# Kernel tuning notes

Measured on AMD Instinct MI355X. Metric: run time of the kernel, lower is better.

## Reference

```python
import jax, jax.numpy as jnp
import numpy as np

N = 50000; E = 800000; T = 800000; G = 64
H = 128; IEMB = 128; BAS = 8; NS = 4; NR = 6; OEH = 128; OUT = 1; NB = 4; CUT = 5.0


def envelope(x):
    # exponent=5 -> p=6: 1/x + a*x^5 + b*x^6 + c*x^7 with a=-28, b=48, c=-21
    return 1.0 / x - 28.0 * x**5 + 48.0 * x**6 - 21.0 * x**7


def setup_inputs() -> dict:
    key = jax.random.key(0)
    ks = iter(jax.random.split(key, 80))
    def w(shape, s=0.1):
        return jax.random.normal(next(ks), shape, dtype=jnp.float32) * s
    inp = {}
    inp['z'] = jax.random.randint(next(ks), (N,), 0, 100, dtype=jnp.int32)
    inp['dist'] = jax.random.uniform(next(ks), (E,), jnp.float32, 0.05, 1.0)
    inp['dist_trip'] = jax.random.uniform(next(ks), (T,), jnp.float32, 0.05, 1.0)
    inp['angle'] = jax.random.uniform(next(ks), (T,), jnp.float32, -1.0, 1.0)
    inp['edge_index'] = jax.random.randint(next(ks), (2, E), 0, N, dtype=jnp.int32)
    inp['triplets'] = jax.random.randint(next(ks), (T, 3), 0, N, dtype=jnp.int32)
    inp['batch'] = jnp.sort(jax.random.randint(next(ks), (N,), 0, G, dtype=jnp.int32))
    inp['atom_table'] = w((100, H), 1.0)
    inp['rbf_freq'] = jnp.arange(1, NR + 1, dtype=jnp.float32) * jnp.float32(np.pi)
    inp['sbf_freq'] = jnp.arange(1, NR + 1, dtype=jnp.float32) * jnp.float32(np.pi)
    inp['emb_w1'] = w((NR, IEMB)); inp['emb_b1'] = w((IEMB,), 0.01)
    inp['emb_w2'] = w((IEMB, H)); inp['emb_b2'] = w((H,), 0.01)
    inp['iw_rbf1'] = w((NB, NR, BAS)); inp['iw_rbf2'] = w((NB, BAS, H))
    inp['iw_sbf1'] = w((NB, NS * NR, BAS)); inp['iw_sbf2'] = w((NB, BAS, IEMB))
    inp['iw_t1'] = w((NB, H, IEMB)); inp['iw_t2'] = w((NB, IEMB, H)); inp['ib_t2'] = w((NB, H), 0.01)
    inp['iw_up'] = w((NB, H, H)); inp['ib_up'] = w((NB, H), 0.01)
    inp['iw_down'] = w((NB, H, H)); inp['ib_down'] = w((NB, H), 0.01)
    inp['ow_rbf'] = w((NB + 1, NR, H))
    inp['ow0'] = w((NB + 1, H, OEH)); inp['ob0'] = w((NB + 1, OEH), 0.01)
    inp['ow1'] = w((NB + 1, OEH, OEH)); inp['ob1'] = w((NB + 1, OEH), 0.01)
    inp['ow2'] = w((NB + 1, OEH, OUT)); inp['ob2'] = w((NB + 1, OUT), 0.01)
    return inp


def _forward(atom_table, rbf_freq, sbf_freq, emb_w1, emb_b1, emb_w2, emb_b2,
             iw_rbf1, iw_rbf2, iw_sbf1, iw_sbf2, iw_t1, iw_t2, ib_t2,
             iw_up, ib_up, iw_down, ib_down, ow_rbf, ow0, ob0, ow1, ob1, ow2, ob2,
             dist, dist_trip, angle, z, edge_index, triplets, batch):
    row, col = edge_index[0], edge_index[1]
    j_idx = triplets[:, 1]
    # radial basis for edges: [E, NR]
    d = dist[:, None] / CUT
    rbf_e = envelope(d) * jnp.sin(rbf_freq * d)
    # spherical basis for triplets: [T, NS*NR]
    dt = dist_trip[:, None] / CUT
    rbf_t = envelope(dt) * jnp.sin(sbf_freq * dt)
    a = angle[:, None]
    sph = jnp.concatenate([jnp.ones_like(a), a, 0.5 * (3 * a**2 - 1), 0.5 * (5 * a**3 - 3 * a)], axis=-1)
    sbf_t = (rbf_t[:, None, :] * sph[:, :, None]).reshape(a.shape[0], -1)

    x = atom_table[z]  # [N, H]
    # EmbeddingBlock: edge msg from rbf only, scattered to col
    e = jax.nn.silu(rbf_e @ emb_w1 + emb_b1) @ emb_w2 + emb_b2
    x = x + jax.ops.segment_sum(e, col, num_segments=N)

    def out_block(k, x):
        rbf_emb = rbf_e @ ow_rbf[k]            # [E, H]
        h = jax.ops.segment_sum(x[row] * rbf_emb, col, num_segments=N)
        h = jax.nn.silu(h @ ow0[k] + ob0[k])
        h = jax.nn.silu(h @ ow1[k] + ob1[k])
        return h @ ow2[k] + ob2[k]             # [N, OUT]

    P = out_block(0, x)
    for b in range(NB):
        x_up = x @ iw_up[b] + ib_up[b]
        x_down = x @ iw_down[b] + ib_down[b]
        rbf_emb = jax.nn.silu(rbf_e @ iw_rbf1[b]) @ iw_rbf2[b]      # [E, H]
        x_edge = x_up[row] * rbf_emb                                  # [E, H]
        sbf_emb = jax.nn.silu(sbf_t @ iw_sbf1[b]) @ iw_sbf2[b]      # [T, H]
        t = jax.nn.silu(x_down @ iw_t1[b]) @ iw_t2[b] + ib_t2[b]     # [N, H]
        # original: for each triplet i, x_edge += t[j]*sbf_emb[i] (broadcast over all edges)
        extra = jnp.sum(t[j_idx] * sbf_emb, axis=0)                   # [H]
        x_edge = x_edge + extra
        x = x + jax.ops.segment_sum(x_edge, col, num_segments=N)
        P = P + out_block(b + 1, x)

    counts = jax.ops.segment_sum(jnp.ones((x.shape[0],), jnp.float32), batch, num_segments=G)
    pooled = jax.ops.segment_sum(P, batch, num_segments=G) / jnp.maximum(counts, 1.0)[:, None]
    return pooled  # [G, OUT]


def reference(z, dist, dist_trip, angle, edge_index, triplets, batch, atom_table, rbf_freq, sbf_freq,
              emb_w1, emb_b1, emb_w2, emb_b2, iw_rbf1, iw_rbf2, iw_sbf1, iw_sbf2, iw_t1, iw_t2, ib_t2,
              iw_up, ib_up, iw_down, ib_down, ow_rbf, ow0, ob0, ow1, ob1, ow2, ob2):
    return _forward(atom_table, rbf_freq, sbf_freq, emb_w1, emb_b1, emb_w2, emb_b2,
                    iw_rbf1, iw_rbf2, iw_sbf1, iw_sbf2, iw_t1, iw_t2, ib_t2,
                    iw_up, ib_up, iw_down, ib_down, ow_rbf, ow0, ob0, ow1, ob1, ow2, ob2,
                    dist, dist_trip, angle, z, edge_index, triplets, batch)
```

## Files before the change

### kernel.cpp

```cpp
#include <hip/hip_runtime.h>
#include <hip/hip_fp16.h>

#define N_ 50000
#define E_ 800000
#define T_ 800000
#define G_ 64
#define H_ 128

#define NBK 782
#define NSB (NBK * 8)
#define CAPS 512

typedef __attribute__((ext_vector_type(8))) short bf16x8;
typedef __attribute__((ext_vector_type(4))) float f32x4;
typedef _Float16 f16x2 __attribute__((ext_vector_type(2)));

__device__ __forceinline__ float siluf(float v) {
    return __fdividef(v, 1.0f + __expf(-v));
}

__device__ __forceinline__ unsigned short f2bf(float f) {
    unsigned int u = __float_as_uint(f);
    u += 0x7fffu + ((u >> 16) & 1u);
    return (unsigned short)(u >> 16);
}
__device__ __forceinline__ unsigned int f2bf2(float a, float b) {
    return (unsigned int)f2bf(a) | ((unsigned int)f2bf(b) << 16);
}
__device__ __forceinline__ float bf2f(unsigned short h) {
    return __uint_as_float(((unsigned int)h) << 16);
}
__device__ __forceinline__ float2 bf2x2(unsigned int p) {
    return make_float2(__uint_as_float(p << 16), __uint_as_float(p & 0xffff0000u));
}
__device__ __forceinline__ float fdot2f(f16x2 a, f16x2 b, float c) {
    return __builtin_amdgcn_fdot2(a, b, c, false);
}

__global__ __launch_bounds__(256) void k_bucket(const int* __restrict__ ecol, const int* __restrict__ erow,
                                                const float* __restrict__ dist,
                                                const int* __restrict__ trip,
                                                const float* __restrict__ dist_trip, const float* __restrict__ angle,
                                                int* bcntE, int2* __restrict__ ebktP, unsigned char* __restrict__ ebktC,
                                                int* bcntT, float2* __restrict__ tbktP, unsigned char* __restrict__ tbktC) {
    int i = blockIdx.x * 256 + threadIdx.x;
    int r = blockIdx.x & 7;
    if (i < E_) {
        int col = ecol[i];
        int sb = (col >> 6) * 8 + r;
        int pos = atomicAdd(&bcntE[sb], 1);
        if (pos < CAPS) {
            ebktP[(size_t)sb * CAPS + pos] = make_int2(erow[i], __float_as_int(dist[i]));
            ebktC[(size_t)sb * CAPS + pos] = (unsigned char)(col & 63);
        }
    }
    int t = i - E_;
    if (t >= 0 && t < T_) {
        int j = trip[3 * t + 1];
        int sb = (j >> 6) * 8 + r;
        int pos = atomicAdd(&bcntT[sb], 1);
        if (pos < CAPS) {
            tbktP[(size_t)sb * CAPS + pos] = make_float2(dist_trip[t], angle[t]);
            tbktC[(size_t)sb * CAPS + pos] = (unsigned char)(j & 63);
        }
    }
}

__global__ __launch_bounds__(256) void k_cnt(const int* __restrict__ bcntE, const unsigned char* __restrict__ ebktC,
                                             const int* __restrict__ bcntT, const unsigned char* __restrict__ tbktC,
                                             int* __restrict__ degE, int* __restrict__ degT) {
    int b = blockIdx.x;
    bool isE = b < NBK;
    if (!isE) b -= NBK;
    __shared__ int c[64];
    int tid = threadIdx.x;
    if (tid < 64) c[tid] = 0;
    __syncthreads();
    const int* bcnt = isE ? bcntE : bcntT;
    const unsigned char* bc = isE ? ebktC : tbktC;
    for (int s = 0; s < 8; ++s) {
        int sb = b * 8 + s;
        int nb = min(bcnt[sb], CAPS);
        for (int i = tid; i < nb; i += 256) atomicAdd(&c[bc[(size_t)sb * CAPS + i]], 1);
    }
    __syncthreads();
    if (tid < 64) {
        int col = b * 64 + tid;
        if (col < N_) (isE ? degE : degT)[col] = c[tid];
    }
}

__global__ __launch_bounds__(1024) void k_scan2(const int* __restrict__ degE, int* rowptrE, int* curE,
                                                const int* __restrict__ degT, int* rowptrT, int* curT, int n) {
    const int* deg = (blockIdx.x == 0) ? degE : degT;
    int* rowptr = (blockIdx.x == 0) ? rowptrE : rowptrT;
    int* cur = (blockIdx.x == 0) ? curE : curT;
    __shared__ int wsum[16];
    __shared__ int s_carry;
    int tid = threadIdx.x, lane = tid & 63, w = tid >> 6;
    if (tid == 0) s_carry = 0;
    __syncthreads();
    for (int base = 0; base < n; base += 1024) {
        int i = base + tid;
        int v = (i < n) ? deg[i] : 0;
        int incl = v;
        #pragma unroll
        for (int s = 1; s < 64; s <<= 1) {
            int t = __shfl_up(incl, (unsigned)s, 64);
            if (lane >= s) incl += t;
        }
        if (lane == 63) wsum[w] = incl;
        __syncthreads();
        int carry0 = s_carry;
        int wexcl = 0;
        for (int j = 0; j < w; ++j) wexcl += wsum[j];
        int excl = carry0 + wexcl + (incl - v);
        if (i < n) { rowptr[i] = excl; cur[i] = excl; }
        __syncthreads();
        if (tid == 1023) s_carry = carry0 + wexcl + incl;
        __syncthreads();
    }
    if (tid == 0) rowptr[n] = s_carry;
}

__global__ __launch_bounds__(256) void k_place(const int* __restrict__ bcntE, const int2* __restrict__ ebktP,
                                               const unsigned char* __restrict__ ebktC, int* curE,
                                               int* __restrict__ slist, float* __restrict__ distS,
                                               const int* __restrict__ bcntT, const float2* __restrict__ tbktP,
                                               const unsigned char* __restrict__ tbktC, int* curT,
                                               float2* __restrict__ tpay) {
    int b = blockIdx.x;
    bool isE = b < NBK;
    if (!isE) b -= NBK;
    int tid = threadIdx.x;
    if (isE) {
        for (int s = 0; s < 8; ++s) {
            int sb = b * 8 + s;
            int nb = min(bcntE[sb], CAPS);
            for (int i = tid; i < nb; i += 256) {
                size_t idx = (size_t)sb * CAPS + i;
                int col = b * 64 + ebktC[idx];
                int2 pr = ebktP[idx];
                int pos = atomicAdd(&curE[col], 1);
                slist[pos] = pr.x;
                distS[pos] = __int_as_float(pr.y);
            }
        }
    } else {
        for (int s = 0; s < 8; ++s) {
            int sb = b * 8 + s;
            int nb = min(bcntT[sb], CAPS);
            for (int i = tid; i < nb; i += 256) {
                size_t idx = (size_t)sb * CAPS + i;
                int col = b * 64 + tbktC[idx];
                float2 pr = tbktP[idx];
                int pos = atomicAdd(&curT[col], 1);
                tpay[pos] = pr;
            }
        }
    }
}

__global__ __launch_bounds__(256) void k_wprep(const float* __restrict__ emb_w2, const float* __restrict__ iw_down,
                                               const float* __restrict__ iw_t1, const float* __restrict__ iw_t2,
                                               const float* __restrict__ iw_up, const float* __restrict__ ow0,
                                               const float* __restrict__ ow1, unsigned short* __restrict__ Wt) {
    int mat = blockIdx.x >> 3;
    int part = blockIdx.x & 7;
    const float* src;
    if (mat == 0) src = emb_w2;
    else if (mat < 5) src = iw_down + (size_t)(mat - 1) * 16384;
    else if (mat < 9) src = iw_t1 + (size_t)(mat - 5) * 16384;
    else if (mat < 13) src = iw_t2 + (size_t)(mat - 9) * 16384;
    else if (mat < 17) src = iw_up + (size_t)(mat - 13) * 16384;
    else if (mat < 22) src = ow0 + (size_t)(mat - 17) * 16384;
    else src = ow1 + (size_t)(mat - 22) * 16384;
    unsigned short* dst = Wt + (size_t)mat * 16384;
    int base = part * 2048;
    for (int i = base + threadIdx.x; i < base + 2048; i += 256) {
        int k = i >> 7, n = i & 127;
        dst[n * 128 + k] = f2bf(src[i]);
    }
}

__global__ __launch_bounds__(256) void k_geom(const float* __restrict__ distS,
                                              const float* __restrict__ freq, const float* __restrict__ iw_rbf1,
                                              float* __restrict__ rbfS, __half* __restrict__ s8all, int n) {
    __shared__ float W1s[4][48];
    int tid = threadIdx.x;
    if (tid < 192) W1s[tid / 48][tid % 48] = iw_rbf1[tid];
    __syncthreads();
    int p = blockIdx.x * 256 + tid;
    if (p >= n) return;
    float d = distS[p] * 0.2f;
    float d2 = d * d, d4 = d2 * d2, d5 = d4 * d;
    float env = __fdividef(1.0f, d) - 28.0f * d5 + 48.0f * d5 * d - 21.0f * d5 * d2;
    float rb[6];
    #pragma unroll
    for (int r = 0; r < 6; ++r) {
        rb[r] = env * __sinf(freq[r] * d);
        rbfS[(size_t)p * 6 + r] = rb[r];
    }
    #pragma unroll
    for (int b = 0; b < 4; ++b) {
        __half out[8];
        #pragma unroll
        for (int k = 0; k < 8; ++k) {
            float u = 0.f;
            #pragma unroll
            for (int r = 0; r < 6; ++r) u += rb[r] * W1s[b][r * 8 + k];
            out[k] = __float2half(siluf(u));
        }
        *(uint4*)&s8all[((size_t)b * n + p) * 8] = *(uint4*)out;
    }
}

__global__ __launch_bounds__(256) void k_basis(const float2* __restrict__ tpay,
                                               const float* __restrict__ sfreq, __half* __restrict__ basis, int n) {
    int t = blockIdx.x * 256 + threadIdx.x;
    if (t >= n) return;
    float2 da = tpay[t];
    float d = da.x * 0.2f;
    float a = da.y;
    float d2 = d * d, d4 = d2 * d2, d5 = d4 * d;
    float env = __fdividef(1.0f, d) - 28.0f * d5 + 48.0f * d5 * d - 21.0f * d5 * d2;
    float rb[6];
    #pragma unroll
    for (int r = 0; r < 6; ++r) rb[r] = env * __sinf(sfreq[r] * d);
    float sph[4];
    sph[0] = 1.0f; sph[1] = a; sph[2] = 1.5f * a * a - 0.5f; sph[3] = 2.5f * a * a * a - 1.5f * a;
    __half out[24];
    #pragma unroll
    for (int s = 0; s < 4; ++s)
        #pragma unroll
        for (int r = 0; r < 6; ++r) out[s * 6 + r] = __float2half(sph[s] * rb[r]);
    uint4* dst = (uint4*)(basis + (size_t)t * 24);
    dst[0] = ((uint4*)out)[0];
    dst[1] = ((uint4*)out)[1];
    dst[2] = ((uint4*)out)[2];
}

__global__ __launch_bounds__(256) void k_sv4(const int* __restrict__ rowptrT, const __half* __restrict__ basis,
                                             const float* __restrict__ iw_sbf1, float* __restrict__ SV4, int n) {
    int wave = threadIdx.x >> 6, lane = threadIdx.x & 63;
    int node = blockIdx.x * 8 + wave * 2 + (lane >> 5);
    int sub = lane & 31;
    int blk = sub >> 3, k = sub & 7;
    if (node >= n) return;
    const float* W1 = iw_sbf1 + blk * 192;
    f16x2 w[12];
    #pragma unroll
    for (int j = 0; j < 12; ++j) {
        f16x2 t;
        t.x = (_Float16)W1[(2 * j) * 8 + k];
        t.y = (_Float16)W1[(2 * j + 1) * 8 + k];
        w[j] = t;
    }
    float acc = 0.f;
    int p0 = rowptrT[node], p1 = rowptrT[node + 1];
    for (int p = p0; p < p1; ++p) {
        union { uint4 q[3]; f16x2 h[12]; } bs;
        const uint4* bp = (const uint4*)(basis + (size_t)p * 24);
        bs.q[0] = bp[0]; bs.q[1] = bp[1]; bs.q[2] = bp[2];
        float u = 0.f;
        #pragma unroll
        for (int j = 0; j < 12; ++j) u = fdot2f(bs.h[j], w[j], u);
        acc += siluf(u);
    }
    SV4[((size_t)blk * n + node) * 8 + k] = acc;
}

__global__ __launch_bounds__(256) void k_init_x(const float* __restrict__ atab, const int* __restrict__ z,
                                                unsigned short* __restrict__ xh, int n) {
    int t = blockIdx.x * 256 + threadIdx.x;
    if (t >= n * 16) return;
    int node = t >> 4, q = t & 15;
    const float4* a4 = (const float4*)atab;
    float4 v0 = a4[(size_t)z[node] * 32 + q * 2];
    float4 v1 = a4[(size_t)z[node] * 32 + q * 2 + 1];
    uint4 pk;
    pk.x = f2bf2(v0.x, v0.y);
    pk.y = f2bf2(v0.z, v0.w);
    pk.z = f2bf2(v1.x, v1.y);
    pk.w = f2bf2(v1.z, v1.w);
    ((uint4*)xh)[t] = pk;
}

__global__ __launch_bounds__(256) void k_embS(const int* __restrict__ rowptr, const float* __restrict__ rbfS,
                                              const float* __restrict__ w1, const float* __restrict__ b1,
                                              float* __restrict__ SS, int n) {
    int node = blockIdx.x * 4 + (threadIdx.x >> 6);
    int lane = threadIdx.x & 63;
    if (node >= n) return;
    int c = lane * 2;
    float wc0[6], wc1[6];
    #pragma unroll
    for (int r = 0; r < 6; ++r) { wc0[r] = w1[r * 128 + c]; wc1[r] = w1[r * 128 + c + 1]; }
    float bb0 = b1[c], bb1 = b1[c + 1];
    float a0 = 0.f, a1 = 0.f;
    int p0 = rowptr[node], p1 = rowptr[node + 1];
    for (int p = p0; p < p1; ++p) {
        const float2* r2 = (const float2*)&rbfS[(size_t)p * 6];
        float2 ra = r2[0], rbx = r2[1], rc = r2[2];
        float u0 = bb0 + ra.x * wc0[0] + ra.y * wc0[1] + rbx.x * wc0[2] + rbx.y * wc0[3] + rc.x * wc0[4] + rc.y * wc0[5];
        float u1 = bb1 + ra.x * wc1[0] + ra.y * wc1[1] + rbx.x * wc1[2] + rbx.y * wc1[3] + rc.x * wc1[4] + rc.y * wc1[5];
        a0 += siluf(u0);
        a1 += siluf(u1);
    }
    SS[node * 128 + c] = a0;
    SS[node * 128 + c + 1] = a1;
}

template <int BIAS_MODE, bool SILU, bool ACCBF, bool ABF, bool WF32, bool WBF>
__global__ __launch_bounds__(256, 4) void k_gemm_mfma(const void* __restrict__ Ap,
                                                      const unsigned short* __restrict__ Wt,
                                                      const float* __restrict__ bias, const int* __restrict__ deg,
                                                      float* __restrict__ C, unsigned short* __restrict__ Ch, int M) {
    int tid = threadIdx.x;
    int wave = tid >> 6, lane = tid & 63;
    int m15 = lane & 15, quad = lane >> 4;
    int row0 = blockIdx.x * 64 + wave * 16;
    int arow = row0 + m15;
    if (arow > M - 1) arow = M - 1;

    f32x4 acc[8];
    #pragma unroll
    for (int nt = 0; nt < 8; ++nt) acc[nt] = (f32x4){0.f, 0.f, 0.f, 0.f};

    #pragma unroll
    for (int kt = 0; kt < 4; ++kt) {
        int ks = kt * 32 + quad * 8;
        bf16x8 av;
        if constexpr (ABF) {
            av = *(const bf16x8*)((const unsigned short*)Ap + (size_t)arow * 128 + ks);
        } else {
            const float* Arow = (const float*)Ap + (size_t)arow * 128;
            float4 a0 = *(const float4*)(Arow + ks);
            float4 a1 = *(const float4*)(Arow + ks + 4);
            union { bf16x8 v; unsigned int u[4]; } af;
            af.u[0] = f2bf2(a0.x, a0.y);
            af.u[1] = f2bf2(a0.z, a0.w);
            af.u[2] = f2bf2(a1.x, a1.y);
            af.u[3] = f2bf2(a1.z, a1.w);
            av = af.v;
        }
        #pragma unroll
        for (int nt = 0; nt < 8; ++nt) {
            bf16x8 bf = *(const bf16x8*)(Wt + (size_t)(nt * 16 + m15) * 128 + ks);
            acc[nt] = __builtin_amdgcn_mfma_f32_16x16x32_bf16(av, bf, acc[nt], 0, 0, 0);
        }
    }

    #pragma unroll
    for (int nt = 0; nt < 8; ++nt) {
        int col = nt * 16 + m15;
        float bc = 0.f;
        if constexpr (BIAS_MODE != 0) bc = bias[col];
        #pragma unroll
        for (int reg = 0; reg < 4; ++reg) {
            int row = row0 + quad * 4 + reg;
            if (row < M) {
                float v = acc[nt][reg];
                if constexpr (BIAS_MODE == 1) v += bc;
                if constexpr (BIAS_MODE == 2) v += bc * (float)deg[row];
                if constexpr (SILU) v = siluf(v);
                if constexpr (ACCBF) v += bf2f(Ch[(size_t)row * 128 + col]);
                if constexpr (WF32) C[(size_t)row * 128 + col] = v;
                if constexpr (WBF) Ch[(size_t)row * 128 + col] = f2bf(v);
            }
        }
    }
}

template <int PACC>
__global__ __launch_bounds__(256, 4) void k_out_mlp(const unsigned short* __restrict__ hB,
                                                    const unsigned short* __restrict__ W0t, const float* __restrict__ b0,
                                                    const unsigned short* __restrict__ W1t, const float* __restrict__ b1,
                                                    const float* __restrict__ w2col, const float* __restrict__ ob2p,
                                                    float* __restrict__ Pout, int M) {
    __shared__ unsigned short lds[4][16 * 136];
    int tid = threadIdx.x;
    int wave = tid >> 6, lane = tid & 63;
    int m15 = lane & 15, quad = lane >> 4;
    int row0 = blockIdx.x * 64 + wave * 16;
    int arow = row0 + m15;
    if (arow > M - 1) arow = M - 1;
    unsigned short* L = lds[wave];

    f32x4 acc[8];
    #pragma unroll
    for (int nt = 0; nt < 8; ++nt) acc[nt] = (f32x4){0.f, 0.f, 0.f, 0.f};
    #pragma unroll
    for (int kt = 0; kt < 4; ++kt) {
        int ks = kt * 32 + quad * 8;
        bf16x8 av = *(const bf16x8*)(hB + (size_t)arow * 128 + ks);
        #pragma unroll
        for (int nt = 0; nt < 8; ++nt) {
            bf16x8 bf = *(const bf16x8*)(W0t + (size_t)(nt * 16 + m15) * 128 + ks);
            acc[nt] = __builtin_amdgcn_mfma_f32_16x16x32_bf16(av, bf, acc[nt], 0, 0, 0);
        }
    }
    #pragma unroll
    for (int nt = 0; nt < 8; ++nt) {
        int col = nt * 16 + m15;
        float bc = b0[col];
        #pragma unroll
        for (int reg = 0; reg < 4; ++reg)
            L[(quad * 4 + reg) * 136 + col] = f2bf(siluf(acc[nt][reg] + bc));
    }
    __syncthreads();

    #pragma unroll
    for (int nt = 0; nt < 8; ++nt) acc[nt] = (f32x4){0.f, 0.f, 0.f, 0.f};
    #pragma unroll
    for (int kt = 0; kt < 4; ++kt) {
        int ks = kt * 32 + quad * 8;
        bf16x8 av = *(const bf16x8*)(L + m15 * 136 + ks);
        #pragma unroll
        for (int nt = 0; nt < 8; ++nt) {
            bf16x8 bf = *(const bf16x8*)(W1t + (size_t)(nt * 16 + m15) * 128 + ks);
            acc[nt] = __builtin_amdgcn_mfma_f32_16x16x32_bf16(av, bf, acc[nt], 0, 0, 0);
        }
    }
    float w2c[8], pp[4];
    #pragma unroll
    for (int nt = 0; nt < 8; ++nt) w2c[nt] = w2col[nt * 16 + m15];
    #pragma unroll
    for (int reg = 0; reg < 4; ++reg) pp[reg] = 0.f;
    #pragma unroll
    for (int nt = 0; nt < 8; ++nt) {
        float bc = b1[nt * 16 + m15];
        #pragma unroll
        for (int reg = 0; reg < 4; ++reg)
            pp[reg] += siluf(acc[nt][reg] + bc) * w2c[nt];
    }
    #pragma unroll
    for (int reg = 0; reg < 4; ++reg) {
        float s = pp[reg];
        s += __shfl_xor(s, 1, 64);
        s += __shfl_xor(s, 2, 64);
        s += __shfl_xor(s, 4, 64);
        s += __shfl_xor(s, 8, 64);
        if (m15 == 0) {
            int row = row0 + quad * 4 + reg;
            if (row < M) {
                float r = s + ob2p[0];
                if constexpr (PACC == 2) r += Pout[row];
                Pout[row] = r;
            }
        }
    }
}

__global__ __launch_bounds__(256, 4) void k_block_mlp(const unsigned short* __restrict__ xh,
                                                      const unsigned short* __restrict__ Wd, const float* __restrict__ bd,
                                                      const unsigned short* __restrict__ Wt1,
                                                      const unsigned short* __restrict__ Wt2, const float* __restrict__ bt2,
                                                      const unsigned short* __restrict__ Wup, const float* __restrict__ bup,
                                                      float* __restrict__ Tm, unsigned short* __restrict__ xuph, int M) {
    __shared__ unsigned short lds[4][16 * 136];
    int tid = threadIdx.x;
    int wave = tid >> 6, lane = tid & 63;
    int m15 = lane & 15, quad = lane >> 4;
    int row0 = blockIdx.x * 64 + wave * 16;
    int arow = row0 + m15;
    if (arow > M - 1) arow = M - 1;
    unsigned short* L = lds[wave];

    f32x4 accD[8], accU[8];
    #pragma unroll
    for (int nt = 0; nt < 8; ++nt) { accD[nt] = (f32x4){0.f, 0.f, 0.f, 0.f}; accU[nt] = (f32x4){0.f, 0.f, 0.f, 0.f}; }
    #pragma unroll
    for (int kt = 0; kt < 4; ++kt) {
        int ks = kt * 32 + quad * 8;
        bf16x8 av = *(const bf16x8*)(xh + (size_t)arow * 128 + ks);
        #pragma unroll
        for (int nt = 0; nt < 8; ++nt) {
            bf16x8 bd_ = *(const bf16x8*)(Wd + (size_t)(nt * 16 + m15) * 128 + ks);
            accD[nt] = __builtin_amdgcn_mfma_f32_16x16x32_bf16(av, bd_, accD[nt], 0, 0, 0);
            bf16x8 bu_ = *(const bf16x8*)(Wup + (size_t)(nt * 16 + m15) * 128 + ks);
            accU[nt] = __builtin_amdgcn_mfma_f32_16x16x32_bf16(av, bu_, accU[nt], 0, 0, 0);
        }
    }
    #pragma unroll
    for (int nt = 0; nt < 8; ++nt) {
        int col = nt * 16 + m15;
        float bcu = bup[col], bcd = bd[col];
        #pragma unroll
        for (int reg = 0; reg < 4; ++reg) {
            int row = row0 + quad * 4 + reg;
            if (row < M) xuph[(size_t)row * 128 + col] = f2bf(accU[nt][reg] + bcu);
            L[(quad * 4 + reg) * 136 + col] = f2bf(accD[nt][reg] + bcd);
        }
    }
    __syncthreads();

    #pragma unroll
    for (int nt = 0; nt < 8; ++nt) accD[nt] = (f32x4){0.f, 0.f, 0.f, 0.f};
    #pragma unroll
    for (int kt = 0; kt < 4; ++kt) {
        int ks = kt * 32 + quad * 8;
        bf16x8 av = *(const bf16x8*)(L + m15 * 136 + ks);
        #pragma unroll
        for (int nt = 0; nt < 8; ++nt) {
            bf16x8 bf = *(const bf16x8*)(Wt1 + (size_t)(nt * 16 + m15) * 128 + ks);
            accD[nt] = __builtin_amdgcn_mfma_f32_16x16x32_bf16(av, bf, accD[nt], 0, 0, 0);
        }
    }
    __syncthreads();
    #pragma unroll
    for (int nt = 0; nt < 8; ++nt) {
        int col = nt * 16 + m15;
        #pragma unroll
        for (int reg = 0; reg < 4; ++reg)
            L[(quad * 4 + reg) * 136 + col] = f2bf(siluf(accD[nt][reg]));
    }
    __syncthreads();

    #pragma unroll
    for (int nt = 0; nt < 8; ++nt) accD[nt] = (f32x4){0.f, 0.f, 0.f, 0.f};
    #pragma unroll
    for (int kt = 0; kt < 4; ++kt) {
        int ks = kt * 32 + quad * 8;
        bf16x8 av = *(const bf16x8*)(L + m15 * 136 + ks);
        #pragma unroll
        for (int nt = 0; nt < 8; ++nt) {
            bf16x8 bf = *(const bf16x8*)(Wt2 + (size_t)(nt * 16 + m15) * 128 + ks);
            accD[nt] = __builtin_amdgcn_mfma_f32_16x16x32_bf16(av, bf, accD[nt], 0, 0, 0);
        }
    }
    #pragma unroll
    for (int nt = 0; nt < 8; ++nt) {
        int col = nt * 16 + m15;
        float bc = bt2[col];
        #pragma unroll
        for (int reg = 0; reg < 4; ++reg) {
            int row = row0 + quad * 4 + reg;
            if (row < M) Tm[(size_t)row * 128 + col] = accD[nt][reg] + bc;
        }
    }
}

__global__ __launch_bounds__(256) void k_out_gather(const int* __restrict__ rowptr, const int* __restrict__ slist,
                                                    const float* __restrict__ rbfS,
                                                    const unsigned short* __restrict__ xh,
                                                    const float* __restrict__ wrbf,
                                                    unsigned short* __restrict__ hB, int n) {
    int node = blockIdx.x * 4 + (threadIdx.x >> 6);
    int lane = threadIdx.x & 63;
    if (node >= n) return;
    int c = lane * 2;
    float wc0[6], wc1[6];
    #pragma unroll
    for (int r = 0; r < 6; ++r) { wc0[r] = wrbf[r * 128 + c]; wc1[r] = wrbf[r * 128 + c + 1]; }
    float a0 = 0.f, a1 = 0.f;
    int p0 = rowptr[node], p1 = rowptr[node + 1];
    int p = p0;
    for (; p + 4 <= p1; p += 4) {
        int s0 = slist[p], s1 = slist[p + 1], s2 = slist[p + 2], s3 = slist[p + 3];
        float2 rb[4][3];
        #pragma unroll
        for (int u = 0; u < 4; ++u) {
            const float2* r2 = (const float2*)&rbfS[(size_t)(p + u) * 6];
            rb[u][0] = r2[0]; rb[u][1] = r2[1]; rb[u][2] = r2[2];
        }
        unsigned int xv0 = *(const unsigned int*)&xh[(size_t)s0 * 128 + c];
        unsigned int xv1 = *(const unsigned int*)&xh[(size_t)s1 * 128 + c];
        unsigned int xv2 = *(const unsigned int*)&xh[(size_t)s2 * 128 + c];
        unsigned int xv3 = *(const unsigned int*)&xh[(size_t)s3 * 128 + c];
        #pragma unroll
        for (int u = 0; u < 4; ++u) {
            float e0 = rb[u][0].x * wc0[0] + rb[u][0].y * wc0[1] + rb[u][1].x * wc0[2] +
                       rb[u][1].y * wc0[3] + rb[u][2].x * wc0[4] + rb[u][2].y * wc0[5];
            float e1 = rb[u][0].x * wc1[0] + rb[u][0].y * wc1[1] + rb[u][1].x * wc1[2] +
                       rb[u][1].y * wc1[3] + rb[u][2].x * wc1[4] + rb[u][2].y * wc1[5];
            float2 xf = bf2x2((u == 0) ? xv0 : (u == 1) ? xv1 : (u == 2) ? xv2 : xv3);
            a0 += xf.x * e0;
            a1 += xf.y * e1;
        }
    }
    for (; p < p1; ++p) {
        int src = slist[p];
        const float2* r2 = (const float2*)&rbfS[(size_t)p * 6];
        float2 ra = r2[0], rbx = r2[1], rc = r2[2];
        float e0 = ra.x * wc0[0] + ra.y * wc0[1] + rbx.x * wc0[2] + rbx.y * wc0[3] + rc.x * wc0[4] + rc.y * wc0[5];
        float e1 = ra.x * wc1[0] + ra.y * wc1[1] + rbx.x * wc1[2] + rbx.y * wc1[3] + rc.x * wc1[4] + rc.y * wc1[5];
        float2 xf = bf2x2(*(const unsigned int*)&xh[(size_t)src * 128 + c]);
        a0 += xf.x * e0;
        a1 += xf.y * e1;
    }
    *(unsigned int*)&hB[(size_t)node * 128 + c] = f2bf2(a0, a1);
}

__global__ __launch_bounds__(256) void k_extra_fused(const float* __restrict__ Tm, const float* __restrict__ SV,
                                                     const float* __restrict__ W2, float* __restrict__ extra, int n) {
    int tid = threadIdx.x;
    int c = tid & 127, half = tid >> 7;
    float acc[8];
    #pragma unroll
    for (int k = 0; k < 8; ++k) acc[k] = 0.f;
    for (int nn = blockIdx.x * 2 + half; nn < n; nn += gridDim.x * 2) {
        const float4* sv4 = (const float4*)&SV[(size_t)nn * 8];
        float4 s0 = sv4[0], s1 = sv4[1];
        float t = Tm[(size_t)nn * 128 + c];
        acc[0] += t * s0.x; acc[1] += t * s0.y; acc[2] += t * s0.z; acc[3] += t * s0.w;
        acc[4] += t * s1.x; acc[5] += t * s1.y; acc[6] += t * s1.z; acc[7] += t * s1.w;
    }
    float e = 0.f;
    #pragma unroll
    for (int k = 0; k < 8; ++k) e += acc[k] * W2[k * 128 + c];
    __shared__ float red[256];
    red[tid] = e;
    __syncthreads();
    if (tid < 128) atomicAdd(&extra[c], red[tid] + red[tid + 128]);
}

__global__ __launch_bounds__(256) void k_interact(const int* __restrict__ rowptr, const int* __restrict__ slist,
                                                  const __half* __restrict__ s8, const float* __restrict__ W2,
                                                  const float* __restrict__ extra,
                                                  const unsigned short* __restrict__ xuph,
                                                  unsigned short* __restrict__ xh, int n) {
    int node = blockIdx.x * 4 + (threadIdx.x >> 6);
    int lane = threadIdx.x & 63;
    if (node >= n) return;
    int c = lane * 2;
    f16x2 w2a[4], w2b[4];
    #pragma unroll
    for (int j = 0; j < 4; ++j) {
        f16x2 wa, wb;
        wa.x = (_Float16)W2[(2 * j) * 128 + c];
        wa.y = (_Float16)W2[(2 * j + 1) * 128 + c];
        wb.x = (_Float16)W2[(2 * j) * 128 + c + 1];
        wb.y = (_Float16)W2[(2 * j + 1) * 128 + c + 1];
        w2a[j] = wa;
        w2b[j] = wb;
    }
    int p0 = rowptr[node], p1 = rowptr[node + 1];
    float cntf = (float)(p1 - p0);
    float a0 = cntf * extra[c], a1 = cntf * extra[c + 1];
    int p = p0;
    for (; p + 4 <= p1; p += 4) {
        int s0 = slist[p], s1 = slist[p + 1], s2 = slist[p + 2], s3 = slist[p + 3];
        uint4 sv[4];
        #pragma unroll
        for (int u = 0; u < 4; ++u) sv[u] = *(const uint4*)(s8 + (size_t)(p + u) * 8);
        unsigned int xv0 = *(const unsigned int*)&xuph[(size_t)s0 * 128 + c];
        unsigned int xv1 = *(const unsigned int*)&xuph[(size_t)s1 * 128 + c];
        unsigned int xv2 = *(const unsigned int*)&xuph[(size_t)s2 * 128 + c];
        unsigned int xv3 = *(const unsigned int*)&xuph[(size_t)s3 * 128 + c];
        #pragma unroll
        for (int u = 0; u < 4; ++u) {
            union { uint4 q; f16x2 h[4]; } s;
            s.q = sv[u];
            float e0 = fdot2f(s.h[0], w2a[0], 0.f);
            e0 = fdot2f(s.h[1], w2a[1], e0);
            e0 = fdot2f(s.h[2], w2a[2], e0);
            e0 = fdot2f(s.h[3], w2a[3], e0);
            float e1 = fdot2f(s.h[0], w2b[0], 0.f);
            e1 = fdot2f(s.h[1], w2b[1], e1);
            e1 = fdot2f(s.h[2], w2b[2], e1);
            e1 = fdot2f(s.h[3], w2b[3], e1);
            float2 xf = bf2x2((u == 0) ? xv0 : (u == 1) ? xv1 : (u == 2) ? xv2 : xv3);
            a0 += xf.x * e0;
            a1 += xf.y * e1;
        }
    }
    for (; p < p1; ++p) {
        int src = slist[p];
        float2 xf = bf2x2(*(const unsigned int*)&xuph[(size_t)src * 128 + c]);
        union { uint4 q; f16x2 h[4]; } s;
        s.q = *(const uint4*)(s8 + (size_t)p * 8);
        float e0 = fdot2f(s.h[0], w2a[0], 0.f);
        e0 = fdot2f(s.h[1], w2a[1], e0);
        e0 = fdot2f(s.h[2], w2a[2], e0);
        e0 = fdot2f(s.h[3], w2a[3], e0);
        float e1 = fdot2f(s.h[0], w2b[0], 0.f);
        e1 = fdot2f(s.h[1], w2b[1], e1);
        e1 = fdot2f(s.h[2], w2b[2], e1);
        e1 = fdot2f(s.h[3], w2b[3], e1);
        a0 += xf.x * e0;
        a1 += xf.y * e1;
    }
    unsigned int cur = *(unsigned int*)&xh[(size_t)node * 128 + c];
    float2 xc = bf2x2(cur);
    *(unsigned int*)&xh[(size_t)node * 128 + c] = f2bf2(xc.x + a0, xc.y + a1);
}

__global__ __launch_bounds__(256) void k_pool(const float* __restrict__ P, const int* __restrict__ batch,
                                              float* __restrict__ pool, float* __restrict__ cnt, int n) {
    int i = blockIdx.x * 256 + threadIdx.x;
    int lane = threadIdx.x & 63;
    int b = (i < n) ? batch[i] : -1;
    float p = (i < n) ? P[i] : 0.f;
    int b0 = __shfl(b, 0, 64);
    int b63 = __shfl(b, 63, 64);
    if (b0 == b63 && b0 >= 0) {
        float s = p;
        #pragma unroll
        for (int off = 32; off > 0; off >>= 1) s += __shfl_xor(s, off, 64);
        if (lane == 0) {
            atomicAdd(&pool[b0], s);
            atomicAdd(&cnt[b0], 64.0f);
        }
    } else {
        if (i < n) {
            atomicAdd(&pool[b], p);
            atomicAdd(&cnt[b], 1.0f);
        }
    }
}

__global__ __launch_bounds__(64) void k_final(const float* __restrict__ pool, const float* __restrict__ cnt,
                                              float* __restrict__ out) {
    int g = threadIdx.x;
    if (g < G_) out[g] = __fdividef(pool[g], fmaxf(cnt[g], 1.0f));
}

extern "C" void kernel_launch(void* const* d_in, const int* in_sizes, int n_in,
                              void* d_out, int out_size, void* d_ws, size_t ws_size,
                              hipStream_t stream) {
    (void)in_sizes; (void)n_in; (void)out_size; (void)ws_size;
    const int* z = (const int*)d_in[0];
    const float* dist = (const float*)d_in[1];
    const float* dist_trip = (const float*)d_in[2];
    const float* angle = (const float*)d_in[3];
    const int* edge_index = (const int*)d_in[4];
    const int* triplets = (const int*)d_in[5];
    const int* batch = (const int*)d_in[6];
    const float* atom_table = (const float*)d_in[7];
    const float* rbf_freq = (const float*)d_in[8];
    const float* sbf_freq = (const float*)d_in[9];
    const float* emb_w1 = (const float*)d_in[10];
    const float* emb_b1 = (const float*)d_in[11];
    const float* emb_w2 = (const float*)d_in[12];
    const float* emb_b2 = (const float*)d_in[13];
    const float* iw_rbf1 = (const float*)d_in[14];
    const float* iw_rbf2 = (const float*)d_in[15];
    const float* iw_sbf1 = (const float*)d_in[16];
    const float* iw_sbf2 = (const float*)d_in[17];
    const float* iw_t1 = (const float*)d_in[18];
    const float* iw_t2 = (const float*)d_in[19];
    const float* ib_t2 = (const float*)d_in[20];
    const float* iw_up = (const float*)d_in[21];
    const float* ib_up = (const float*)d_in[22];
    const float* iw_down = (const float*)d_in[23];
    const float* ib_down = (const float*)d_in[24];
    const float* ow_rbf = (const float*)d_in[25];
    const float* ow0 = (const float*)d_in[26];
    const float* ob0 = (const float*)d_in[27];
    const float* ow1 = (const float*)d_in[28];
    const float* ob1 = (const float*)d_in[29];
    const float* ow2 = (const float*)d_in[30];
    const float* ob2 = (const float*)d_in[31];

    const int* erow = edge_index;
    const int* ecol = edge_index + E_;

    float* ws = (float*)d_ws;
    float* bufA = ws;
    float* bufB = bufA + (size_t)N_ * H_;
    float* P = bufB + (size_t)N_ * H_;
    float* rbfS = P + N_;
    float* SV4 = rbfS + (size_t)E_ * 6;
    float* extra4 = SV4 + (size_t)4 * N_ * 8;
    float* pool = extra4 + 512;
    float* cnt = pool + G_;
    int* bcntE = (int*)(cnt + G_);
    int* bcntT = bcntE + NSB;
    int* degE = bcntT + NSB;
    int* degT = degE + N_;
    int* rowptr = degT + N_;
    int* curE = rowptr + N_ + 1;
    int* curT = curE + N_;
    int* slist = curT + N_;
    int* rowptrT = slist + E_;
    float* distS = (float*)(rowptrT + N_ + 1);
    uintptr_t tp = (uintptr_t)(distS + E_);
    tp = (tp + 7) & ~(uintptr_t)7;
    float2* tpay = (float2*)tp;
    __half* s8all = (__half*)(tpay + T_);
    __half* basis = s8all + (size_t)4 * E_ * 8;
    unsigned short* xh = (unsigned short*)(basis + (size_t)T_ * 24);
    unsigned short* xuph = xh + (size_t)N_ * H_;
    unsigned short* Wt = xuph + (size_t)N_ * H_;
    unsigned short* hB = (unsigned short*)bufB;

    int2* ebktP = (int2*)s8all;
    unsigned char* ebktC = (unsigned char*)(ebktP + (size_t)NSB * CAPS);
    float2* tbktP = (float2*)(ebktC + (size_t)NSB * CAPS);
    unsigned char* tbktC = (unsigned char*)(tbktP + (size_t)NSB * CAPS);

    const int EG = (E_ + 255) / 256;
    const int TG = (T_ + 255) / 256;
    const int ETG = (E_ + T_ + 255) / 256;
    const int NG4 = (N_ + 3) / 4;
    const int GEMMG = (N_ + 63) / 64;

    hipMemsetAsync(extra4, 0, (512 + 2 * G_ + 2 * NSB) * sizeof(float), stream);
    k_wprep<<<27 * 8, 256, 0, stream>>>(emb_w2, iw_down, iw_t1, iw_t2, iw_up, ow0, ow1, Wt);
    k_bucket<<<ETG, 256, 0, stream>>>(ecol, erow, dist, triplets, dist_trip, angle,
                                      bcntE, ebktP, ebktC, bcntT, tbktP, tbktC);
    k_cnt<<<2 * NBK, 256, 0, stream>>>(bcntE, ebktC, bcntT, tbktC, degE, degT);
    k_scan2<<<2, 1024, 0, stream>>>(degE, rowptr, curE, degT, rowptrT, curT, N_);
    k_place<<<2 * NBK, 256, 0, stream>>>(bcntE, ebktP, ebktC, curE, slist, distS,
                                         bcntT, tbktP, tbktC, curT, tpay);

    k_geom<<<EG, 256, 0, stream>>>(distS, rbf_freq, iw_rbf1, rbfS, s8all, E_);
    k_basis<<<TG, 256, 0, stream>>>(tpay, sbf_freq, basis, T_);
    k_sv4<<<(N_ + 7) / 8, 256, 0, stream>>>(rowptrT, basis, iw_sbf1, SV4, N_);
    k_init_x<<<(N_ * 16 + 255) / 256, 256, 0, stream>>>(atom_table, z, xh, N_);

    k_embS<<<NG4, 256, 0, stream>>>(rowptr, rbfS, emb_w1, emb_b1, bufA, N_);
    k_gemm_mfma<2, false, true, false, false, true><<<GEMMG, 256, 0, stream>>>(
        bufA, Wt, emb_b2, degE, nullptr, xh, N_);

    auto out_block = [&](int k, bool first) {
        k_out_gather<<<NG4, 256, 0, stream>>>(rowptr, slist, rbfS, xh,
                                              ow_rbf + (size_t)k * 6 * 128, hB, N_);
        if (first)
            k_out_mlp<1><<<GEMMG, 256, 0, stream>>>(hB, Wt + (size_t)(17 + k) * 16384, ob0 + k * 128,
                                                    Wt + (size_t)(22 + k) * 16384, ob1 + k * 128,
                                                    ow2 + k * 128, ob2 + k, P, N_);
        else
            k_out_mlp<2><<<GEMMG, 256, 0, stream>>>(hB, Wt + (size_t)(17 + k) * 16384, ob0 + k * 128,
                                                    Wt + (size_t)(22 + k) * 16384, ob1 + k * 128,
                                                    ow2 + k * 128, ob2 + k, P, N_);
    };

    out_block(0, true);

    for (int b = 0; b < 4; ++b) {
        k_block_mlp<<<GEMMG, 256, 0, stream>>>(xh,
                                               Wt + (size_t)(1 + b) * 16384, ib_down + b * 128,
                                               Wt + (size_t)(5 + b) * 16384,
                                               Wt + (size_t)(9 + b) * 16384, ib_t2 + b * 128,
                                               Wt + (size_t)(13 + b) * 16384, ib_up + b * 128,
                                               bufA, xuph, N_);
        k_extra_fused<<<256, 256, 0, stream>>>(bufA, SV4 + (size_t)b * N_ * 8,
                                               iw_sbf2 + (size_t)b * 1024, extra4 + b * 128, N_);
        k_interact<<<NG4, 256, 0, stream>>>(rowptr, slist, s8all + (size_t)b * E_ * 8,
                                            iw_rbf2 + (size_t)b * 1024, extra4 + b * 128,
                                            xuph, xh, N_);
        out_block(b + 1, false);
    }

    k_pool<<<(N_ + 255) / 256, 256, 0, stream>>>(P, batch, pool, cnt, N_);
    k_final<<<1, 64, 0, stream>>>(pool, cnt, (float*)d_out);
}
```

Baseline: 1.697 ms.

## Fuse extra reduction into block MLP, slim bucket records, bf16 embedding input

```diff
diff --git a/kernel.cpp b/kernel.cpp
--- a/kernel.cpp
+++ b/kernel.cpp
@@ -37,12 +37,10 @@
     return __builtin_amdgcn_fdot2(a, b, c, false);
 }
 
-__global__ __launch_bounds__(256) void k_bucket(const int* __restrict__ ecol, const int* __restrict__ erow,
-                                                const float* __restrict__ dist,
+__global__ __launch_bounds__(256) void k_bucket(const int* __restrict__ ecol,
                                                 const int* __restrict__ trip,
-                                                const float* __restrict__ dist_trip, const float* __restrict__ angle,
-                                                int* bcntE, int2* __restrict__ ebktP, unsigned char* __restrict__ ebktC,
-                                                int* bcntT, float2* __restrict__ tbktP, unsigned char* __restrict__ tbktC) {
+                                                int* bcntE, unsigned int* __restrict__ ebkt, int* __restrict__ degE,
+                                                int* bcntT, unsigned int* __restrict__ tbkt, int* __restrict__ degT) {
     int i = blockIdx.x * 256 + threadIdx.x;
     int r = blockIdx.x & 7;
     if (i < E_) {
@@ -50,8 +48,8 @@
         int sb = (col >> 6) * 8 + r;
         int pos = atomicAdd(&bcntE[sb], 1);
         if (pos < CAPS) {
-            ebktP[(size_t)sb * CAPS + pos] = make_int2(erow[i], __float_as_int(dist[i]));
-            ebktC[(size_t)sb * CAPS + pos] = (unsigned char)(col & 63);
+            ebkt[(size_t)sb * CAPS + pos] = ((unsigned int)i << 6) | (unsigned int)(col & 63);
+            atomicAdd(&degE[col], 1);
         }
     }
     int t = i - E_;
@@ -60,33 +58,9 @@
         int sb = (j >> 6) * 8 + r;
         int pos = atomicAdd(&bcntT[sb], 1);
         if (pos < CAPS) {
-            tbktP[(size_t)sb * CAPS + pos] = make_float2(dist_trip[t], angle[t]);
-            tbktC[(size_t)sb * CAPS + pos] = (unsigned char)(j & 63);
-        }
-    }
-}
-
-__global__ __launch_bounds__(256) void k_cnt(const int* __restrict__ bcntE, const unsigned char* __restrict__ ebktC,
-                                             const int* __restrict__ bcntT, const unsigned char* __restrict__ tbktC,
-                                             int* __restrict__ degE, int* __restrict__ degT) {
-    int b = blockIdx.x;
-    bool isE = b < NBK;
-    if (!isE) b -= NBK;
-    __shared__ int c[64];
-    int tid = threadIdx.x;
-    if (tid < 64) c[tid] = 0;
-    __syncthreads();
-    const int* bcnt = isE ? bcntE : bcntT;
-    const unsigned char* bc = isE ? ebktC : tbktC;
-    for (int s = 0; s < 8; ++s) {
-        int sb = b * 8 + s;
-        int nb = min(bcnt[sb], CAPS);
-        for (int i = tid; i < nb; i += 256) atomicAdd(&c[bc[(size_t)sb * CAPS + i]], 1);
-    }
-    __syncthreads();
-    if (tid < 64) {
-        int col = b * 64 + tid;
-        if (col < N_) (isE ? degE : degT)[col] = c[tid];
+            tbkt[(size_t)sb * CAPS + pos] = ((unsigned int)t << 6) | (unsigned int)(j & 63);
+            atomicAdd(&degT[j], 1);
+        }
     }
 }
 
@@ -123,12 +97,12 @@
     if (tid == 0) rowptr[n] = s_carry;
 }
 
-__global__ __launch_bounds__(256) void k_place(const int* __restrict__ bcntE, const int2* __restrict__ ebktP,
-                                               const unsigned char* __restrict__ ebktC, int* curE,
-                                               int* __restrict__ slist, float* __restrict__ distS,
-                                               const int* __restrict__ bcntT, const float2* __restrict__ tbktP,
-                                               const unsigned char* __restrict__ tbktC, int* curT,
-                                               float2* __restrict__ tpay) {
+__global__ __launch_bounds__(256) void k_place(const int* __restrict__ bcntE, const unsigned int* __restrict__ ebkt,
+                                               const int* __restrict__ erow, const float* __restrict__ dist,
+                                               int* curE, int* __restrict__ slist, float* __restrict__ distS,
+                                               const int* __restrict__ bcntT, const unsigned int* __restrict__ tbkt,
+                                               const float* __restrict__ dist_trip, const float* __restrict__ angle,
+                                               int* curT, float2* __restrict__ tpay) {
     int b = blockIdx.x;
     bool isE = b < NBK;
     if (!isE) b -= NBK;
@@ -138,12 +112,12 @@
             int sb = b * 8 + s;
             int nb = min(bcntE[sb], CAPS);
             for (int i = tid; i < nb; i += 256) {
-                size_t idx = (size_t)sb * CAPS + i;
-                int col = b * 64 + ebktC[idx];
-                int2 pr = ebktP[idx];
+                unsigned int rec = ebkt[(size_t)sb * CAPS + i];
+                int e = (int)(rec >> 6);
+                int col = b * 64 + (int)(rec & 63u);
                 int pos = atomicAdd(&curE[col], 1);
-                slist[pos] = pr.x;
-                distS[pos] = __int_as_float(pr.y);
+                slist[pos] = erow[e];
+                distS[pos] = dist[e];
             }
         }
     } else {
@@ -151,11 +125,11 @@
             int sb = b * 8 + s;
             int nb = min(bcntT[sb], CAPS);
             for (int i = tid; i < nb; i += 256) {
-                size_t idx = (size_t)sb * CAPS + i;
-                int col = b * 64 + tbktC[idx];
-                float2 pr = tbktP[idx];
+                unsigned int rec = tbkt[(size_t)sb * CAPS + i];
+                int t = (int)(rec >> 6);
+                int col = b * 64 + (int)(rec & 63u);
                 int pos = atomicAdd(&curT[col], 1);
-                tpay[pos] = pr;
+                tpay[pos] = make_float2(dist_trip[t], angle[t]);
             }
         }
     }
@@ -288,7 +262,7 @@
 
 __global__ __launch_bounds__(256) void k_embS(const int* __restrict__ rowptr, const float* __restrict__ rbfS,
                                               const float* __restrict__ w1, const float* __restrict__ b1,
-                                              float* __restrict__ SS, int n) {
+                                              unsigned short* __restrict__ SSh, int n) {
     int node = blockIdx.x * 4 + (threadIdx.x >> 6);
     int lane = threadIdx.x & 63;
     if (node >= n) return;
@@ -307,8 +281,7 @@
         a0 += siluf(u0);
         a1 += siluf(u1);
     }
-    SS[node * 128 + c] = a0;
-    SS[node * 128 + c + 1] = a1;
+    *(unsigned int*)&SSh[(size_t)node * 128 + c] = f2bf2(a0, a1);
 }
 
 template <int BIAS_MODE, bool SILU, bool ACCBF, bool ABF, bool WF32, bool WBF>
@@ -457,15 +430,20 @@
                                                       const unsigned short* __restrict__ Wt1,
                                                       const unsigned short* __restrict__ Wt2, const float* __restrict__ bt2,
                                                       const unsigned short* __restrict__ Wup, const float* __restrict__ bup,
-                                                      float* __restrict__ Tm, unsigned short* __restrict__ xuph, int M) {
-    __shared__ unsigned short lds[4][16 * 136];
+                                                      const float* __restrict__ SV, const float* __restrict__ W2,
+                                                      float* __restrict__ extra,
+                                                      unsigned short* __restrict__ xuph, int M) {
+    __shared__ union {
+        unsigned short h[4][16 * 136];
+        float f[64 * 132];
+    } sm;
     int tid = threadIdx.x;
     int wave = tid >> 6, lane = tid & 63;
     int m15 = lane & 15, quad = lane >> 4;
     int row0 = blockIdx.x * 64 + wave * 16;
     int arow = row0 + m15;
     if (arow > M - 1) arow = M - 1;
-    unsigned short* L = lds[wave];
+    unsigned short* L = sm.h[wave];
 
     f32x4 accD[8], accU[8];
     #pragma unroll
@@ -529,16 +507,39 @@
             accD[nt] = __builtin_amdgcn_mfma_f32_16x16x32_bf16(av, bf, accD[nt], 0, 0, 0);
         }
     }
+    __syncthreads();
     #pragma unroll
     for (int nt = 0; nt < 8; ++nt) {
         int col = nt * 16 + m15;
         float bc = bt2[col];
         #pragma unroll
         for (int reg = 0; reg < 4; ++reg) {
-            int row = row0 + quad * 4 + reg;
-            if (row < M) Tm[(size_t)row * 128 + col] = accD[nt][reg] + bc;
-        }
-    }
+            int lr = wave * 16 + quad * 4 + reg;
+            sm.f[lr * 132 + col] = accD[nt][reg] + bc;
+        }
+    }
+    __syncthreads();
+
+    int col = tid & 127, half = tid >> 7;
+    float acc8[8];
+    #pragma unroll
+    for (int k = 0; k < 8; ++k) acc8[k] = 0.f;
+    int rmax = M - blockIdx.x * 64;
+    if (rmax > 64) rmax = 64;
+    for (int rr = half; rr < rmax; rr += 2) {
+        float t = sm.f[rr * 132 + col];
+        const float4* sv4 = (const float4*)&SV[(size_t)(blockIdx.x * 64 + rr) * 8];
+        float4 s0 = sv4[0], s1 = sv4[1];
+        acc8[0] += t * s0.x; acc8[1] += t * s0.y; acc8[2] += t * s0.z; acc8[3] += t * s0.w;
+        acc8[4] += t * s1.x; acc8[5] += t * s1.y; acc8[6] += t * s1.z; acc8[7] += t * s1.w;
+    }
+    float e = 0.f;
+    #pragma unroll
+    for (int k = 0; k < 8; ++k) e += acc8[k] * W2[k * 128 + col];
+    __syncthreads();
+    sm.f[tid] = e;
+    __syncthreads();
+    if (tid < 128) atomicAdd(&extra[col], sm.f[tid] + sm.f[tid + 128]);
 }
 
 __global__ __launch_bounds__(256) void k_out_gather(const int* __restrict__ rowptr, const int* __restrict__ slist,
@@ -590,29 +591,6 @@
         a1 += xf.y * e1;
     }
     *(unsigned int*)&hB[(size_t)node * 128 + c] = f2bf2(a0, a1);
-}
-
-__global__ __launch_bounds__(256) void k_extra_fused(const float* __restrict__ Tm, const float* __restrict__ SV,
-                                                     const float* __restrict__ W2, float* __restrict__ extra, int n) {
-    int tid = threadIdx.x;
-    int c = tid & 127, half = tid >> 7;
-    float acc[8];
-    #pragma unroll
-    for (int k = 0; k < 8; ++k) acc[k] = 0.f;
-    for (int nn = blockIdx.x * 2 + half; nn < n; nn += gridDim.x * 2) {
-        const float4* sv4 = (const float4*)&SV[(size_t)nn * 8];
-        float4 s0 = sv4[0], s1 = sv4[1];
-        float t = Tm[(size_t)nn * 128 + c];
-        acc[0] += t * s0.x; acc[1] += t * s0.y; acc[2] += t * s0.z; acc[3] += t * s0.w;
-        acc[4] += t * s1.x; acc[5] += t * s1.y; acc[6] += t * s1.z; acc[7] += t * s1.w;
-    }
-    float e = 0.f;
-    #pragma unroll
-    for (int k = 0; k < 8; ++k) e += acc[k] * W2[k * 128 + c];
-    __shared__ float red[256];
-    red[tid] = e;
-    __syncthreads();
-    if (tid < 128) atomicAdd(&extra[c], red[tid] + red[tid + 128]);
 }
 
 __global__ __launch_bounds__(256) void k_interact(const int* __restrict__ rowptr, const int* __restrict__ slist,
@@ -785,10 +763,8 @@
     unsigned short* Wt = xuph + (size_t)N_ * H_;
     unsigned short* hB = (unsigned short*)bufB;
 
-    int2* ebktP = (int2*)s8all;
-    unsigned char* ebktC = (unsigned char*)(ebktP + (size_t)NSB * CAPS);
-    float2* tbktP = (float2*)(ebktC + (size_t)NSB * CAPS);
-    unsigned char* tbktC = (unsigned char*)(tbktP + (size_t)NSB * CAPS);
+    unsigned int* ebkt = (unsigned int*)s8all;
+    unsigned int* tbkt = ebkt + (size_t)NSB * CAPS;
 
     const int EG = (E_ + 255) / 256;
     const int TG = (T_ + 255) / 256;
@@ -796,22 +772,20 @@
     const int NG4 = (N_ + 3) / 4;
     const int GEMMG = (N_ + 63) / 64;
 
-    hipMemsetAsync(extra4, 0, (512 + 2 * G_ + 2 * NSB) * sizeof(float), stream);
+    hipMemsetAsync(extra4, 0, (512 + 2 * G_ + 2 * NSB + 2 * N_) * sizeof(float), stream);
     k_wprep<<<27 * 8, 256, 0, stream>>>(emb_w2, iw_down, iw_t1, iw_t2, iw_up, ow0, ow1, Wt);
-    k_bucket<<<ETG, 256, 0, stream>>>(ecol, erow, dist, triplets, dist_trip, angle,
-                                      bcntE, ebktP, ebktC, bcntT, tbktP, tbktC);
-    k_cnt<<<2 * NBK, 256, 0, stream>>>(bcntE, ebktC, bcntT, tbktC, degE, degT);
+    k_bucket<<<ETG, 256, 0, stream>>>(ecol, triplets, bcntE, ebkt, degE, bcntT, tbkt, degT);
     k_scan2<<<2, 1024, 0, stream>>>(degE, rowptr, curE, degT, rowptrT, curT, N_);
-    k_place<<<2 * NBK, 256, 0, stream>>>(bcntE, ebktP, ebktC, curE, slist, distS,
-                                         bcntT, tbktP, tbktC, curT, tpay);
+    k_place<<<2 * NBK, 256, 0, stream>>>(bcntE, ebkt, erow, dist, curE, slist, distS,
+                                         bcntT, tbkt, dist_trip, angle, curT, tpay);
 
     k_geom<<<EG, 256, 0, stream>>>(distS, rbf_freq, iw_rbf1, rbfS, s8all, E_);
     k_basis<<<TG, 256, 0, stream>>>(tpay, sbf_freq, basis, T_);
     k_sv4<<<(N_ + 7) / 8, 256, 0, stream>>>(rowptrT, basis, iw_sbf1, SV4, N_);
     k_init_x<<<(N_ * 16 + 255) / 256, 256, 0, stream>>>(atom_table, z, xh, N_);
 
-    k_embS<<<NG4, 256, 0, stream>>>(rowptr, rbfS, emb_w1, emb_b1, bufA, N_);
-    k_gemm_mfma<2, false, true, false, false, true><<<GEMMG, 256, 0, stream>>>(
+    k_embS<<<NG4, 256, 0, stream>>>(rowptr, rbfS, emb_w1, emb_b1, (unsigned short*)bufA, N_);
+    k_gemm_mfma<2, false, true, true, false, true><<<GEMMG, 256, 0, stream>>>(
         bufA, Wt, emb_b2, degE, nullptr, xh, N_);
 
     auto out_block = [&](int k, bool first) {
@@ -835,9 +809,10 @@
                                                Wt + (size_t)(5 + b) * 16384,
                                                Wt + (size_t)(9 + b) * 16384, ib_t2 + b * 128,
                                                Wt + (size_t)(13 + b) * 16384, ib_up + b * 128,
-                                               bufA, xuph, N_);
-        k_extra_fused<<<256, 256, 0, stream>>>(bufA, SV4 + (size_t)b * N_ * 8,
-                                               iw_sbf2 + (size_t)b * 1024, extra4 + b * 128, N_);
+                                               SV4 + (size_t)b * N_ * 8,
+                                               iw_sbf2 + (size_t)b * 1024,
+                                               extra4 + b * 128,
+                                               xuph, N_);
         k_interact<<<NG4, 256, 0, stream>>>(rowptr, slist, s8all + (size_t)b * E_ * 8,
                                             iw_rbf2 + (size_t)b * 1024, extra4 + b * 128,
                                             xuph, xh, N_);
```

New measurement: 1.701 ms. About the same (+0.3%).
